# Performance work log

Hardware: AMD Instinct MI355X
Metric: run time of the kernel (lower is better)

The kernel has to match this reference:

```python
import jax, jax.numpy as jnp
import numpy as np

NT, NC, D = 20000, 80000, 256
SLOPE = 0.01  # torch F.leaky_relu default negative_slope


def _lrelu(x):
    return jnp.where(x >= 0, x, SLOPE * x)


def setup_inputs() -> dict:
    key = jax.random.key(0)
    ks = jax.random.split(key, 20)
    sc = 1.0 / np.sqrt(D)

    def W(k):
        return jax.random.normal(k, (D, D), jnp.float32) * sc

    return {
        "feat_table": jax.random.normal(ks[0], (NT, D), jnp.float32),
        "feat_column": jax.random.normal(ks[1], (NC, D), jnp.float32),
        "W_t2c": W(ks[2]), "b_t2c": jnp.zeros((D,), jnp.float32),
        "W_c2t": W(ks[3]), "b_c2t": jnp.zeros((D,), jnp.float32),
        "W_c2c": W(ks[4]), "b_c2c": jnp.zeros((D,), jnp.float32),
        "W_t2t": W(ks[5]), "b_t2t": jnp.zeros((D,), jnp.float32),
        "W_h": W(ks[6]), "b_h": jnp.zeros((D,), jnp.float32),
        "src_t2c": jax.random.randint(ks[7], (320000,), 0, NT, jnp.int32),
        "dst_t2c": jax.random.randint(ks[8], (320000,), 0, NC, jnp.int32),
        "src_c2t": jax.random.randint(ks[9], (320000,), 0, NC, jnp.int32),
        "dst_c2t": jax.random.randint(ks[10], (320000,), 0, NT, jnp.int32),
        "src_c2c": jax.random.randint(ks[11], (640000,), 0, NC, jnp.int32),
        "dst_c2c": jax.random.randint(ks[12], (640000,), 0, NC, jnp.int32),
        "src_t2t": jax.random.randint(ks[13], (160000,), 0, NT, jnp.int32),
        "dst_t2t": jax.random.randint(ks[14], (160000,), 0, NT, jnp.int32),
    }


def _mean_agg(Wh, src, dst, n_dst):
    # copy_u + mean: gather src messages, segment-mean into dst nodes
    s = jax.ops.segment_sum(Wh[src], dst, num_segments=n_dst)  # [n_dst, D]
    c = jax.ops.segment_sum(jnp.ones(src.shape, Wh.dtype), dst, num_segments=n_dst)
    return s / jnp.maximum(c, 1.0)[:, None]


def reference(feat_table, feat_column,
              W_t2c, b_t2c, W_c2t, b_c2t, W_c2c, b_c2c, W_t2t, b_t2t,
              W_h, b_h,
              src_t2c, dst_t2c, src_c2t, dst_c2t,
              src_c2c, dst_c2c, src_t2t, dst_t2t):
    # per-etype Linear + leaky_relu on source-node features
    Wh_t2c = _lrelu(feat_table @ W_t2c.T + b_t2c)
    Wh_c2t = _lrelu(feat_column @ W_c2t.T + b_c2t)
    Wh_c2c = _lrelu(feat_column @ W_c2c.T + b_c2c)
    Wh_t2t = _lrelu(feat_table @ W_t2t.T + b_t2t)

    # per-etype mean aggregation, then cross-etype 'mean' (2 etypes per ntype)
    h_table = 0.5 * (_mean_agg(Wh_c2t, src_c2t, dst_c2t, NT)
                     + _mean_agg(Wh_t2t, src_t2t, dst_t2t, NT))
    h_column = 0.5 * (_mean_agg(Wh_t2c, src_t2c, dst_t2c, NC)
                      + _mean_agg(Wh_c2c, src_c2c, dst_c2c, NC))

    out_table = _lrelu(h_table @ W_h.T + b_h) + feat_table
    out_column = _lrelu(h_column @ W_h.T + b_h) + feat_column
    return out_table, out_column
```

## Files before the change

kernel.cpp:

```cpp
#include <hip/hip_runtime.h>

#define D 256
#define SLOPE 0.01f

typedef __attribute__((ext_vector_type(8))) short bf16x8;
typedef __attribute__((ext_vector_type(4))) float f32x4;

__device__ __forceinline__ float bfbits2f(unsigned int hi) {
  return __builtin_bit_cast(float, hi);
}
__device__ __forceinline__ unsigned short f2bf(float f) {
  unsigned u = __builtin_bit_cast(unsigned, f);
  u += 0x7fffu + ((u >> 16) & 1u);
  return (unsigned short)(u >> 16);
}
__device__ __forceinline__ float lrelu(float x) {
  return (x >= 0.f) ? x : SLOPE * x;
}

__device__ __forceinline__ void gld_lds16(const void* g, void* l) {
  __builtin_amdgcn_global_load_lds(
      (const __attribute__((address_space(1))) unsigned int*)g,
      (__attribute__((address_space(3))) unsigned int*)l, 16, 0, 0);
}

__global__ void cast_kernel(const float* __restrict__ in,
                            unsigned short* __restrict__ out, int n4) {
  int i = blockIdx.x * blockDim.x + threadIdx.x;
  if (i >= n4) return;
  float4 v = ((const float4*)in)[i];
  ushort4 o;
  o.x = f2bf(v.x); o.y = f2bf(v.y); o.z = f2bf(v.z); o.w = f2bf(v.w);
  ((ushort4*)out)[i] = o;
}

__global__ void cast5_kernel(const float* w0, const float* w1, const float* w2,
                             const float* w3, const float* w4,
                             unsigned short* o0, unsigned short* o1,
                             unsigned short* o2, unsigned short* o3,
                             unsigned short* o4) {
  int a = blockIdx.y;
  const float* in = a == 0 ? w0 : a == 1 ? w1 : a == 2 ? w2 : a == 3 ? w3 : w4;
  unsigned short* out = a == 0 ? o0 : a == 1 ? o1 : a == 2 ? o2 : a == 3 ? o3 : o4;
  int i = blockIdx.x * blockDim.x + threadIdx.x;
  float4 v = ((const float4*)in)[i];
  ushort4 o;
  o.x = f2bf(v.x); o.y = f2bf(v.y); o.z = f2bf(v.z); o.w = f2bf(v.w);
  ((ushort4*)out)[i] = o;
}

template <int MODE>
__global__ __launch_bounds__(256, 2) void gemm_v2(
    const unsigned short* __restrict__ A, const unsigned short* __restrict__ B,
    const float* __restrict__ bias, const float* __restrict__ residual,
    unsigned short* __restrict__ outb, float* __restrict__ outf, int M) {
  __shared__ __attribute__((aligned(16))) unsigned short Xs[64 * 256];
  const int t = threadIdx.x;
  const int w = t >> 6, lane = t & 63;
  const int mblk = blockIdx.x * 64;
  const int fr = lane & 15;
  const int jb = lane >> 4;

  bf16x8 wf[4][8];
  {
    const unsigned short* wp =
        B + (size_t)(w * 64 + fr) * D + jb * 8;
#pragma unroll
    for (int nt = 0; nt < 4; nt++)
#pragma unroll
      for (int k0 = 0; k0 < 8; k0++)
        wf[nt][k0] = *(const bf16x8*)(wp + nt * 16 * D + k0 * 32);
  }

#pragma unroll
  for (int i = 0; i < 8; i++) {
    const int m = (i * 4 + w) * 2 + (lane >> 5);
    int row = mblk + m;
    if (row > M - 1) row = M - 1;
    const int jsrc = (lane & 31) ^ (m & 7);
    gld_lds16(A + (size_t)row * D + jsrc * 8, &Xs[(i * 4 + w) * 512]);
  }
  asm volatile("s_waitcnt vmcnt(0)" ::: "memory");
  __syncthreads();

  f32x4 acc[4][4];
#pragma unroll
  for (int i = 0; i < 4; i++)
#pragma unroll
    for (int j = 0; j < 4; j++) acc[i][j] = (f32x4){0.f, 0.f, 0.f, 0.f};

  const int r = fr & 7;
#pragma unroll
  for (int k0 = 0; k0 < 8; k0++) {
    bf16x8 xf[4];
#pragma unroll
    for (int mt = 0; mt < 4; mt++) {
      const int ml = mt * 16 + fr;
      xf[mt] = *(const bf16x8*)&Xs[ml * 256 + (((k0 * 4 + jb) ^ r) * 8)];
    }
#pragma unroll
    for (int mt = 0; mt < 4; mt++)
#pragma unroll
      for (int nt = 0; nt < 4; nt++)
        acc[mt][nt] = __builtin_amdgcn_mfma_f32_16x16x32_bf16(
            wf[nt][k0], xf[mt], acc[mt][nt], 0, 0, 0);
  }

  const int n0 = w * 64 + jb * 4;
  float4 bv[4];
#pragma unroll
  for (int nt = 0; nt < 4; nt++) bv[nt] = *(const float4*)&bias[n0 + nt * 16];

#pragma unroll
  for (int mt = 0; mt < 4; mt++) {
    const int m = mblk + mt * 16 + fr;
    if (m < M) {
      if (MODE == 1) {
        float4 rv[4];
#pragma unroll
        for (int nt = 0; nt < 4; nt++)
          rv[nt] = *(const float4*)&residual[(size_t)m * D + n0 + nt * 16];
#pragma unroll
        for (int nt = 0; nt < 4; nt++) {
          float4 o;
          o.x = lrelu(acc[mt][nt][0] + bv[nt].x) + rv[nt].x;
          o.y = lrelu(acc[mt][nt][1] + bv[nt].y) + rv[nt].y;
          o.z = lrelu(acc[mt][nt][2] + bv[nt].z) + rv[nt].z;
          o.w = lrelu(acc[mt][nt][3] + bv[nt].w) + rv[nt].w;
          *(float4*)&outf[(size_t)m * D + n0 + nt * 16] = o;
        }
      } else {
#pragma unroll
        for (int nt = 0; nt < 4; nt++) {
          ushort4 o;
          o.x = f2bf(lrelu(acc[mt][nt][0] + bv[nt].x));
          o.y = f2bf(lrelu(acc[mt][nt][1] + bv[nt].y));
          o.z = f2bf(lrelu(acc[mt][nt][2] + bv[nt].z));
          o.w = f2bf(lrelu(acc[mt][nt][3] + bv[nt].w));
          *(ushort4*)&outb[(size_t)m * D + n0 + nt * 16] = o;
        }
      }
    }
  }
}

__global__ void hist4_kernel(const int* d0, int n0, int* c0, const int* d1,
                             int n1, int* c1, const int* d2, int n2, int* c2,
                             const int* d3, int n3, int* c3) {
  int a = blockIdx.y;
  const int* dst = a == 0 ? d0 : a == 1 ? d1 : a == 2 ? d2 : d3;
  int n = a == 0 ? n0 : a == 1 ? n1 : a == 2 ? n2 : n3;
  int* cnt = a == 0 ? c0 : a == 1 ? c1 : a == 2 ? c2 : c3;
  int i = blockIdx.x * blockDim.x + threadIdx.x;
  if (i < n) atomicAdd(&cnt[dst[i]], 1);
}

__global__ __launch_bounds__(256) void scan_p1(
    const int* c0, int n0, const int* c1, int n1, const int* c2, int n2,
    const int* c3, int n3, int* __restrict__ bsum) {
  int a = blockIdx.y;
  const int* cnt = a == 0 ? c0 : a == 1 ? c1 : a == 2 ? c2 : c3;
  int n = a == 0 ? n0 : a == 1 ? n1 : a == 2 ? n2 : n3;
  int nblk = (n + 1023) >> 10;
  int blk = blockIdx.x;
  if (blk >= nblk) return;
  int t = threadIdx.x;
  int i = (blk << 10) + t * 4;
  int s = 0;
  if (i + 3 < n) {
    int4 v = *(const int4*)(cnt + i);
    s = v.x + v.y + v.z + v.w;
  } else {
#pragma unroll
    for (int j = 0; j < 4; j++)
      if (i + j < n) s += cnt[i + j];
  }
  __shared__ int red[256];
  red[t] = s;
  __syncthreads();
  for (int off = 128; off > 0; off >>= 1) {
    if (t < off) red[t] += red[t + off];
    __syncthreads();
  }
  if (t == 0) bsum[a * 128 + blk] = red[0];
}

__global__ __launch_bounds__(128) void scan_p2(int* __restrict__ bsum, int* o0,
                                               int n0, int* o1, int n1, int* o2,
                                               int n2, int* o3, int n3) {
  int a = blockIdx.x;
  int* offs = a == 0 ? o0 : a == 1 ? o1 : a == 2 ? o2 : o3;
  int n = a == 0 ? n0 : a == 1 ? n1 : a == 2 ? n2 : n3;
  int nblk = (n + 1023) >> 10;
  int t = threadIdx.x;
  int v = (t < nblk) ? bsum[a * 128 + t] : 0;
  __shared__ int s[128];
  s[t] = v;
  __syncthreads();
  for (int off = 1; off < 128; off <<= 1) {
    int u = (t >= off) ? s[t - off] : 0;
    __syncthreads();
    s[t] += u;
    __syncthreads();
  }
  if (t < nblk) bsum[a * 128 + t] = s[t] - v;
  if (t == 127) offs[n] = s[127];
}

__global__ __launch_bounds__(256) void scan_p3(
    const int* c0, int* o0, int n0, const int* c1, int* o1, int n1,
    const int* c2, int* o2, int n2, const int* c3, int* o3, int n3,
    const int* __restrict__ bsum) {
  int a = blockIdx.y;
  const int* cnt = a == 0 ? c0 : a == 1 ? c1 : a == 2 ? c2 : c3;
  int* offs = a == 0 ? o0 : a == 1 ? o1 : a == 2 ? o2 : o3;
  int n = a == 0 ? n0 : a == 1 ? n1 : a == 2 ? n2 : n3;
  int nblk = (n + 1023) >> 10;
  int blk = blockIdx.x;
  if (blk >= nblk) return;
  int t = threadIdx.x;
  int i = (blk << 10) + t * 4;
  int4 v = {0, 0, 0, 0};
  if (i + 3 < n) {
    v = *(const int4*)(cnt + i);
  } else {
    if (i < n) v.x = cnt[i];
    if (i + 1 < n) v.y = cnt[i + 1];
    if (i + 2 < n) v.z = cnt[i + 2];
    if (i + 3 < n) v.w = cnt[i + 3];
  }
  int s = v.x + v.y + v.z + v.w;
  __shared__ int sm[256];
  sm[t] = s;
  __syncthreads();
  for (int off = 1; off < 256; off <<= 1) {
    int u = (t >= off) ? sm[t - off] : 0;
    __syncthreads();
    sm[t] += u;
    __syncthreads();
  }
  int ex = sm[t] - s + bsum[a * 128 + blk];
  int4 o;
  o.x = ex;
  o.y = ex + v.x;
  o.z = ex + v.x + v.y;
  o.w = ex + v.x + v.y + v.z;
  if (i + 3 < n) {
    *(int4*)(offs + i) = o;
  } else {
    if (i < n) offs[i] = o.x;
    if (i + 1 < n) offs[i + 1] = o.y;
    if (i + 2 < n) offs[i + 2] = o.z;
    if (i + 3 < n) offs[i + 3] = o.w;
  }
}

__global__ void scatter4_kernel(
    const int* s0, const int* d0, int n0, const int* f0, int* u0, int* e0,
    const int* s1, const int* d1, int n1, const int* f1, int* u1, int* e1,
    const int* s2, const int* d2, int n2, const int* f2, int* u2, int* e2,
    const int* s3, const int* d3, int n3, const int* f3, int* u3, int* e3) {
  int a = blockIdx.y;
  const int* src = a == 0 ? s0 : a == 1 ? s1 : a == 2 ? s2 : s3;
  const int* dst = a == 0 ? d0 : a == 1 ? d1 : a == 2 ? d2 : d3;
  int n = a == 0 ? n0 : a == 1 ? n1 : a == 2 ? n2 : n3;
  const int* offs = a == 0 ? f0 : a == 1 ? f1 : a == 2 ? f2 : f3;
  int* cur = a == 0 ? u0 : a == 1 ? u1 : a == 2 ? u2 : u3;
  int* elist = a == 0 ? e0 : a == 1 ? e1 : a == 2 ? e2 : e3;
  int i = blockIdx.x * blockDim.x + threadIdx.x;
  if (i < n) {
    int d = dst[i];
    int p = offs[d] + atomicAdd(&cur[d], 1);
    elist[p] = src[i];
  }
}

__device__ __forceinline__ void add8(float* acc, uint4 p) {
  acc[0] += bfbits2f(p.x << 16);
  acc[1] += bfbits2f(p.x & 0xffff0000u);
  acc[2] += bfbits2f(p.y << 16);
  acc[3] += bfbits2f(p.y & 0xffff0000u);
  acc[4] += bfbits2f(p.z << 16);
  acc[5] += bfbits2f(p.z & 0xffff0000u);
  acc[6] += bfbits2f(p.w << 16);
  acc[7] += bfbits2f(p.w & 0xffff0000u);
}

__global__ __launch_bounds__(256) void aggregate_kernel(
    const unsigned short* __restrict__ WhA, const int* __restrict__ offsA,
    const int* __restrict__ elistA, const unsigned short* __restrict__ WhB,
    const int* __restrict__ offsB, const int* __restrict__ elistB,
    unsigned short* __restrict__ hout, int n) {
  int wave = (blockIdx.x * 256 + threadIdx.x) >> 6;
  int lane = threadIdx.x & 63;
  if (wave >= n) return;
  int half = lane >> 5;
  int l32 = lane & 31;
  size_t coff = (size_t)l32 * 8;

  float accA[8] = {0, 0, 0, 0, 0, 0, 0, 0};
  float accB[8] = {0, 0, 0, 0, 0, 0, 0, 0};
  float scA, scB;

  {
    int e0 = offsA[wave], e1 = offsA[wave + 1];
    scA = 0.5f / fmaxf((float)(e1 - e0), 1.0f);
    int e = e0;
    for (; e + 8 <= e1; e += 8) {
      int s0 = elistA[e + half];
      int s1 = elistA[e + 2 + half];
      int s2 = elistA[e + 4 + half];
      int s3 = elistA[e + 6 + half];
      uint4 p0 = *(const uint4*)(WhA + (size_t)s0 * D + coff);
      uint4 p1 = *(const uint4*)(WhA + (size_t)s1 * D + coff);
      uint4 p2 = *(const uint4*)(WhA + (size_t)s2 * D + coff);
      uint4 p3 = *(const uint4*)(WhA + (size_t)s3 * D + coff);
      add8(accA, p0); add8(accA, p1); add8(accA, p2); add8(accA, p3);
    }
    for (; e + 2 <= e1; e += 2) {
      int s0 = elistA[e + half];
      uint4 p0 = *(const uint4*)(WhA + (size_t)s0 * D + coff);
      add8(accA, p0);
    }
    if (e < e1 && half == 0) {
      int s0 = elistA[e];
      uint4 p0 = *(const uint4*)(WhA + (size_t)s0 * D + coff);
      add8(accA, p0);
    }
  }
  {
    int e0 = offsB[wave], e1 = offsB[wave + 1];
    scB = 0.5f / fmaxf((float)(e1 - e0), 1.0f);
    int e = e0;
    for (; e + 8 <= e1; e += 8) {
      int s0 = elistB[e + half];
      int s1 = elistB[e + 2 + half];
      int s2 = elistB[e + 4 + half];
      int s3 = elistB[e + 6 + half];
      uint4 p0 = *(const uint4*)(WhB + (size_t)s0 * D + coff);
      uint4 p1 = *(const uint4*)(WhB + (size_t)s1 * D + coff);
      uint4 p2 = *(const uint4*)(WhB + (size_t)s2 * D + coff);
      uint4 p3 = *(const uint4*)(WhB + (size_t)s3 * D + coff);
      add8(accB, p0); add8(accB, p1); add8(accB, p2); add8(accB, p3);
    }
    for (; e + 2 <= e1; e += 2) {
      int s0 = elistB[e + half];
      uint4 p0 = *(const uint4*)(WhB + (size_t)s0 * D + coff);
      add8(accB, p0);
    }
    if (e < e1 && half == 0) {
      int s0 = elistB[e];
      uint4 p0 = *(const uint4*)(WhB + (size_t)s0 * D + coff);
      add8(accB, p0);
    }
  }

  float h[8];
#pragma unroll
  for (int j = 0; j < 8; j++) {
    h[j] = accA[j] * scA + accB[j] * scB;
    h[j] += __shfl_down(h[j], 32);
  }
  if (half == 0) {
    uint4 o;
    o.x = (unsigned)f2bf(h[0]) | ((unsigned)f2bf(h[1]) << 16);
    o.y = (unsigned)f2bf(h[2]) | ((unsigned)f2bf(h[3]) << 16);
    o.z = (unsigned)f2bf(h[4]) | ((unsigned)f2bf(h[5]) << 16);
    o.w = (unsigned)f2bf(h[6]) | ((unsigned)f2bf(h[7]) << 16);
    *(uint4*)(hout + (size_t)wave * D + coff) = o;
  }
}

extern "C" void kernel_launch(void* const* d_in, const int* in_sizes, int n_in,
                              void* d_out, int out_size, void* d_ws,
                              size_t ws_size, hipStream_t stream) {
  const float* feat_table = (const float*)d_in[0];
  const float* feat_column = (const float*)d_in[1];
  const float* Wsrc[5] = {(const float*)d_in[2], (const float*)d_in[4],
                          (const float*)d_in[6], (const float*)d_in[8],
                          (const float*)d_in[10]};
  const float* b_t2c = (const float*)d_in[3];
  const float* b_c2t = (const float*)d_in[5];
  const float* b_c2c = (const float*)d_in[7];
  const float* b_t2t = (const float*)d_in[9];
  const float* b_h = (const float*)d_in[11];
  const int* src_t2c = (const int*)d_in[12];
  const int* dst_t2c = (const int*)d_in[13];
  const int* src_c2t = (const int*)d_in[14];
  const int* dst_c2t = (const int*)d_in[15];
  const int* src_c2c = (const int*)d_in[16];
  const int* dst_c2c = (const int*)d_in[17];
  const int* src_t2t = (const int*)d_in[18];
  const int* dst_t2t = (const int*)d_in[19];

  const int NT = in_sizes[0] / D;
  const int NC = in_sizes[1] / D;
  const int E_t2c = in_sizes[12], E_c2t = in_sizes[14];
  const int E_c2c = in_sizes[16], E_t2t = in_sizes[18];

  char* ws = (char*)d_ws;
  size_t cur = 0;
  auto alloc = [&](size_t bytes) -> void* {
    void* p = ws + cur;
    cur += (bytes + 255) & ~(size_t)255;
    return p;
  };
  unsigned short* Wb[5];
  for (int i = 0; i < 5; i++) Wb[i] = (unsigned short*)alloc((size_t)D * D * 2);
  unsigned short* ftb = (unsigned short*)alloc((size_t)NT * D * 2);
  unsigned short* fcb = (unsigned short*)alloc((size_t)NC * D * 2);
  unsigned short* Wh_t2c = (unsigned short*)alloc((size_t)NT * D * 2);
  unsigned short* Wh_c2t = (unsigned short*)alloc((size_t)NC * D * 2);
  unsigned short* Wh_c2c = (unsigned short*)alloc((size_t)NC * D * 2);
  unsigned short* Wh_t2t = (unsigned short*)alloc((size_t)NT * D * 2);
  unsigned short* h_tab = (unsigned short*)alloc((size_t)NT * D * 2);
  unsigned short* h_col = (unsigned short*)alloc((size_t)NC * D * 2);
  int* ints = (int*)alloc(sizeof(int) * 2 * (2 * (size_t)NT + 2 * (size_t)NC));
  int* cnt_c2t = ints;
  int* cnt_t2t = cnt_c2t + NT;
  int* cnt_t2c = cnt_t2t + NT;
  int* cnt_c2c = cnt_t2c + NC;
  int* cur_c2t = cnt_c2c + NC;
  int* cur_t2t = cur_c2t + NT;
  int* cur_t2c = cur_t2t + NT;
  int* cur_c2c = cur_t2c + NC;
  int* off_c2t = (int*)alloc(sizeof(int) * (NT + 1));
  int* off_t2t = (int*)alloc(sizeof(int) * (NT + 1));
  int* off_t2c = (int*)alloc(sizeof(int) * (NC + 1));
  int* off_c2c = (int*)alloc(sizeof(int) * (NC + 1));
  int* el_c2t = (int*)alloc(sizeof(int) * E_c2t);
  int* el_t2t = (int*)alloc(sizeof(int) * E_t2t);
  int* el_t2c = (int*)alloc(sizeof(int) * E_t2c);
  int* el_c2c = (int*)alloc(sizeof(int) * E_c2c);
  int* bsum = (int*)alloc(sizeof(int) * 4 * 128);

  hipMemsetAsync(ints, 0, sizeof(int) * 2 * (2 * (size_t)NT + 2 * (size_t)NC),
                 stream);

  {
    dim3 g((D * D / 4 + 255) / 256, 5);
    cast5_kernel<<<g, 256, 0, stream>>>(Wsrc[0], Wsrc[1], Wsrc[2], Wsrc[3],
                                        Wsrc[4], Wb[0], Wb[1], Wb[2], Wb[3],
                                        Wb[4]);
  }
  cast_kernel<<<((NT * D / 4) + 255) / 256, 256, 0, stream>>>(feat_table, ftb,
                                                              NT * D / 4);
  cast_kernel<<<((NC * D / 4) + 255) / 256, 256, 0, stream>>>(feat_column, fcb,
                                                              NC * D / 4);

  {
    dim3 g((NT + 63) / 64);
    gemm_v2<0><<<g, 256, 0, stream>>>(ftb, Wb[0], b_t2c, nullptr, Wh_t2c,
                                      nullptr, NT);
    gemm_v2<0><<<g, 256, 0, stream>>>(ftb, Wb[3], b_t2t, nullptr, Wh_t2t,
                                      nullptr, NT);
  }
  {
    dim3 g((NC + 63) / 64);
    gemm_v2<0><<<g, 256, 0, stream>>>(fcb, Wb[1], b_c2t, nullptr, Wh_c2t,
                                      nullptr, NC);
    gemm_v2<0><<<g, 256, 0, stream>>>(fcb, Wb[2], b_c2c, nullptr, Wh_c2c,
                                      nullptr, NC);
  }

  int Emax = max(max(E_c2t, E_t2t), max(E_t2c, E_c2c));
  {
    dim3 g((Emax + 255) / 256, 4);
    hist4_kernel<<<g, 256, 0, stream>>>(dst_c2t, E_c2t, cnt_c2t, dst_t2t,
                                        E_t2t, cnt_t2t, dst_t2c, E_t2c,
                                        cnt_t2c, dst_c2c, E_c2c, cnt_c2c);
  }
  int nmax = max(NT, NC);
  {
    dim3 g((nmax + 1023) / 1024, 4);
    scan_p1<<<g, 256, 0, stream>>>(cnt_c2t, NT, cnt_t2t, NT, cnt_t2c, NC,
                                   cnt_c2c, NC, bsum);
    scan_p2<<<4, 128, 0, stream>>>(bsum, off_c2t, NT, off_t2t, NT, off_t2c, NC,
                                   off_c2c, NC);
    scan_p3<<<g, 256, 0, stream>>>(cnt_c2t, off_c2t, NT, cnt_t2t, off_t2t, NT,
                                   cnt_t2c, off_t2c, NC, cnt_c2c, off_c2c, NC,
                                   bsum);
  }
  {
    dim3 g((Emax + 255) / 256, 4);
    scatter4_kernel<<<g, 256, 0, stream>>>(
        src_c2t, dst_c2t, E_c2t, off_c2t, cur_c2t, el_c2t, src_t2t, dst_t2t,
        E_t2t, off_t2t, cur_t2t, el_t2t, src_t2c, dst_t2c, E_t2c, off_t2c,
        cur_t2c, el_t2c, src_c2c, dst_c2c, E_c2c, off_c2c, cur_c2c, el_c2c);
  }

  aggregate_kernel<<<(NT + 3) / 4, 256, 0, stream>>>(
      Wh_c2t, off_c2t, el_c2t, Wh_t2t, off_t2t, el_t2t, h_tab, NT);
  aggregate_kernel<<<(NC + 3) / 4, 256, 0, stream>>>(
      Wh_t2c, off_t2c, el_t2c, Wh_c2c, off_c2c, el_c2c, h_col, NC);

  float* out_tab = (float*)d_out;
  float* out_col = out_tab + (size_t)NT * D;
  {
    dim3 g((NT + 63) / 64);
    gemm_v2<1><<<g, 256, 0, stream>>>(h_tab, Wb[4], b_h, feat_table, nullptr,
                                      out_tab, NT);
  }
  {
    dim3 g((NC + 63) / 64);
    gemm_v2<1><<<g, 256, 0, stream>>>(h_col, Wb[4], b_h, feat_column, nullptr,
                                      out_col, NC);
  }
}
```

Baseline: 620.0 us.

## Fuse feature cast into dual-weight GEMM and bucket edges before CSR scatter

The first-layer GEMMs now read fp32 features directly, convert them to bf16 in registers and write them to LDS. One 512-thread block computes both etype projections from the same input tile, which removes the separate cast kernels and the reload of the bf16 copy. The CSR edge scatter becomes a two-pass bucketed scheme: edges are first grouped into 512-node buckets using LDS counters, then scattered within each bucket. This localizes the global atomics and the elist writes, at the cost of an extra temp buffer and one more kernel launch.

```diff
diff --git a/kernel.cpp b/kernel.cpp
--- a/kernel.cpp
+++ b/kernel.cpp
@@ -2,6 +2,11 @@
 
 #define D 256
 #define SLOPE 0.01f
+
+#define BSH 9
+#define BSZ 512
+#define NBMAX 160
+#define EPB 8192
 
 typedef __attribute__((ext_vector_type(8))) short bf16x8;
 typedef __attribute__((ext_vector_type(4))) float f32x4;
@@ -22,16 +27,6 @@
   __builtin_amdgcn_global_load_lds(
       (const __attribute__((address_space(1))) unsigned int*)g,
       (__attribute__((address_space(3))) unsigned int*)l, 16, 0, 0);
-}
-
-__global__ void cast_kernel(const float* __restrict__ in,
-                            unsigned short* __restrict__ out, int n4) {
-  int i = blockIdx.x * blockDim.x + threadIdx.x;
-  if (i >= n4) return;
-  float4 v = ((const float4*)in)[i];
-  ushort4 o;
-  o.x = f2bf(v.x); o.y = f2bf(v.y); o.z = f2bf(v.z); o.w = f2bf(v.w);
-  ((ushort4*)out)[i] = o;
 }
 
 __global__ void cast5_kernel(const float* w0, const float* w1, const float* w2,
@@ -49,6 +44,104 @@
   ((ushort4*)out)[i] = o;
 }
 
+__global__ __launch_bounds__(512, 2) void gemm0_dual(
+    const float* __restrict__ Af, const unsigned short* __restrict__ B1,
+    const unsigned short* __restrict__ B2, const float* __restrict__ bias1,
+    const float* __restrict__ bias2, unsigned short* __restrict__ o1,
+    unsigned short* __restrict__ o2, int M) {
+  __shared__ __attribute__((aligned(16))) unsigned short Xs[64 * 256];
+  const int t = threadIdx.x;
+  const int wv = t >> 6, lane = t & 63;
+  const int half = wv >> 2;
+  const int w = wv & 3;
+  const int mblk = blockIdx.x * 64;
+  const int fr = lane & 15;
+  const int jb = lane >> 4;
+
+  const unsigned short* B = half ? B2 : B1;
+  const float* bias = half ? bias2 : bias1;
+  unsigned short* outb = half ? o2 : o1;
+
+  float4 v0[4], v1[4];
+  int cds[4];
+#pragma unroll
+  for (int i = 0; i < 4; i++) {
+    const int c = i * 512 + t;
+    const int m = c >> 5, jg = c & 31;
+    int row = mblk + m;
+    if (row > M - 1) row = M - 1;
+    const float* gp = Af + (size_t)row * D + jg * 8;
+    v0[i] = *(const float4*)gp;
+    v1[i] = *(const float4*)(gp + 4);
+    cds[i] = m * 32 + (jg ^ (m & 7));
+  }
+
+  bf16x8 wf[4][8];
+  {
+    const unsigned short* wp = B + (size_t)(w * 64 + fr) * D + jb * 8;
+#pragma unroll
+    for (int nt = 0; nt < 4; nt++)
+#pragma unroll
+      for (int k0 = 0; k0 < 8; k0++)
+        wf[nt][k0] = *(const bf16x8*)(wp + nt * 16 * D + k0 * 32);
+  }
+
+#pragma unroll
+  for (int i = 0; i < 4; i++) {
+    uint4 pk;
+    pk.x = (unsigned)f2bf(v0[i].x) | ((unsigned)f2bf(v0[i].y) << 16);
+    pk.y = (unsigned)f2bf(v0[i].z) | ((unsigned)f2bf(v0[i].w) << 16);
+    pk.z = (unsigned)f2bf(v1[i].x) | ((unsigned)f2bf(v1[i].y) << 16);
+    pk.w = (unsigned)f2bf(v1[i].z) | ((unsigned)f2bf(v1[i].w) << 16);
+    *(uint4*)&Xs[cds[i] * 8] = pk;
+  }
+  __syncthreads();
+
+  f32x4 acc[4][4];
+#pragma unroll
+  for (int i = 0; i < 4; i++)
+#pragma unroll
+    for (int j = 0; j < 4; j++) acc[i][j] = (f32x4){0.f, 0.f, 0.f, 0.f};
+
+  const int r = fr & 7;
+#pragma unroll
+  for (int k0 = 0; k0 < 8; k0++) {
+    bf16x8 xf[4];
+#pragma unroll
+    for (int mt = 0; mt < 4; mt++) {
+      const int ml = mt * 16 + fr;
+      xf[mt] = *(const bf16x8*)&Xs[ml * 256 + (((k0 * 4 + jb) ^ r) * 8)];
+    }
+#pragma unroll
+    for (int mt = 0; mt < 4; mt++)
+#pragma unroll
+      for (int nt = 0; nt < 4; nt++)
+        acc[mt][nt] = __builtin_amdgcn_mfma_f32_16x16x32_bf16(
+            wf[nt][k0], xf[mt], acc[mt][nt], 0, 0, 0);
+  }
+
+  const int n0 = w * 64 + jb * 4;
+  float4 bv[4];
+#pragma unroll
+  for (int nt = 0; nt < 4; nt++) bv[nt] = *(const float4*)&bias[n0 + nt * 16];
+
+#pragma unroll
+  for (int mt = 0; mt < 4; mt++) {
+    const int m = mblk + mt * 16 + fr;
+    if (m < M) {
+#pragma unroll
+      for (int nt = 0; nt < 4; nt++) {
+        ushort4 o;
+        o.x = f2bf(lrelu(acc[mt][nt][0] + bv[nt].x));
+        o.y = f2bf(lrelu(acc[mt][nt][1] + bv[nt].y));
+        o.z = f2bf(lrelu(acc[mt][nt][2] + bv[nt].z));
+        o.w = f2bf(lrelu(acc[mt][nt][3] + bv[nt].w));
+        *(ushort4*)&outb[(size_t)m * D + n0 + nt * 16] = o;
+      }
+    }
+  }
+}
+
 template <int MODE>
 __global__ __launch_bounds__(256, 2) void gemm_v2(
     const unsigned short* __restrict__ A, const unsigned short* __restrict__ B,
@@ -63,8 +156,7 @@
 
   bf16x8 wf[4][8];
   {
-    const unsigned short* wp =
-        B + (size_t)(w * 64 + fr) * D + jb * 8;
+    const unsigned short* wp = B + (size_t)(w * 64 + fr) * D + jb * 8;
 #pragma unroll
     for (int nt = 0; nt < 4; nt++)
 #pragma unroll
@@ -255,23 +347,85 @@
   }
 }
 
-__global__ void scatter4_kernel(
-    const int* s0, const int* d0, int n0, const int* f0, int* u0, int* e0,
-    const int* s1, const int* d1, int n1, const int* f1, int* u1, int* e1,
-    const int* s2, const int* d2, int n2, const int* f2, int* u2, int* e2,
-    const int* s3, const int* d3, int n3, const int* f3, int* u3, int* e3) {
+__global__ __launch_bounds__(256) void bucketA_kernel(
+    const int* s0, const int* d0, int n0, const int* f0, int* g0, unsigned* t0, int m0,
+    const int* s1, const int* d1, int n1, const int* f1, int* g1, unsigned* t1, int m1,
+    const int* s2, const int* d2, int n2, const int* f2, int* g2, unsigned* t2, int m2,
+    const int* s3, const int* d3, int n3, const int* f3, int* g3, unsigned* t3, int m3) {
   int a = blockIdx.y;
   const int* src = a == 0 ? s0 : a == 1 ? s1 : a == 2 ? s2 : s3;
   const int* dst = a == 0 ? d0 : a == 1 ? d1 : a == 2 ? d2 : d3;
   int n = a == 0 ? n0 : a == 1 ? n1 : a == 2 ? n2 : n3;
-  const int* offs = a == 0 ? f0 : a == 1 ? f1 : a == 2 ? f2 : f3;
+  const int* off = a == 0 ? f0 : a == 1 ? f1 : a == 2 ? f2 : f3;
+  int* bcur = a == 0 ? g0 : a == 1 ? g1 : a == 2 ? g2 : g3;
+  unsigned* temp = a == 0 ? t0 : a == 1 ? t1 : a == 2 ? t2 : t3;
+  int nn = a == 0 ? m0 : a == 1 ? m1 : a == 2 ? m2 : m3;
+
+  int blk = blockIdx.x;
+  if (blk * EPB >= n) return;
+  int nb = (nn + BSZ - 1) >> BSH;
+  int t = threadIdx.x;
+  __shared__ int cnt[NBMAX];
+  __shared__ int lbase[NBMAX];
+  if (t < NBMAX) cnt[t] = 0;
+  __syncthreads();
+
+  int i0 = blk * EPB + t;
+#pragma unroll 4
+  for (int it = 0; it < EPB / 256; it++) {
+    int i = i0 + it * 256;
+    if (i < n) atomicAdd(&cnt[dst[i] >> BSH], 1);
+  }
+  __syncthreads();
+  if (t < nb) {
+    int c = cnt[t];
+    int g = c ? atomicAdd(&bcur[t], c) : 0;
+    lbase[t] = g + off[t << BSH];
+    cnt[t] = 0;
+  }
+  __syncthreads();
+#pragma unroll 4
+  for (int it = 0; it < EPB / 256; it++) {
+    int i = i0 + it * 256;
+    if (i < n) {
+      int d = dst[i];
+      int b = d >> BSH;
+      int rk = atomicAdd(&cnt[b], 1);
+      temp[lbase[b] + rk] = ((unsigned)src[i] << BSH) | (unsigned)(d & (BSZ - 1));
+    }
+  }
+}
+
+__global__ __launch_bounds__(256) void bucketB_kernel(
+    const unsigned* t0, const int* f0, int* u0, int* e0, int m0,
+    const unsigned* t1, const int* f1, int* u1, int* e1, int m1,
+    const unsigned* t2, const int* f2, int* u2, int* e2, int m2,
+    const unsigned* t3, const int* f3, int* u3, int* e3, int m3) {
+  int a = blockIdx.y;
+  const unsigned* temp = a == 0 ? t0 : a == 1 ? t1 : a == 2 ? t2 : t3;
+  const int* off = a == 0 ? f0 : a == 1 ? f1 : a == 2 ? f2 : f3;
   int* cur = a == 0 ? u0 : a == 1 ? u1 : a == 2 ? u2 : u3;
   int* elist = a == 0 ? e0 : a == 1 ? e1 : a == 2 ? e2 : e3;
-  int i = blockIdx.x * blockDim.x + threadIdx.x;
-  if (i < n) {
-    int d = dst[i];
-    int p = offs[d] + atomicAdd(&cur[d], 1);
-    elist[p] = src[i];
+  int nn = a == 0 ? m0 : a == 1 ? m1 : a == 2 ? m2 : m3;
+
+  int nb = (nn + BSZ - 1) >> BSH;
+  int b = blockIdx.x >> 2, q = blockIdx.x & 3;
+  if (b >= nb) return;
+  int lo = off[b << BSH];
+  int hiIdx = (b + 1) << BSH;
+  if (hiIdx > nn) hiIdx = nn;
+  int hi = off[hiIdx];
+  int len = hi - lo;
+  int chunk = (len + 3) >> 2;
+  int st = lo + q * chunk;
+  int en = st + chunk;
+  if (en > hi) en = hi;
+  for (int i = st + threadIdx.x; i < en; i += 256) {
+    unsigned v = temp[i];
+    int d = (b << BSH) | (int)(v & (BSZ - 1));
+    int s = (int)(v >> BSH);
+    int p = off[d] + atomicAdd(&cur[d], 1);
+    elist[p] = s;
   }
 }
 
@@ -407,15 +561,14 @@
   };
   unsigned short* Wb[5];
   for (int i = 0; i < 5; i++) Wb[i] = (unsigned short*)alloc((size_t)D * D * 2);
-  unsigned short* ftb = (unsigned short*)alloc((size_t)NT * D * 2);
-  unsigned short* fcb = (unsigned short*)alloc((size_t)NC * D * 2);
   unsigned short* Wh_t2c = (unsigned short*)alloc((size_t)NT * D * 2);
   unsigned short* Wh_c2t = (unsigned short*)alloc((size_t)NC * D * 2);
   unsigned short* Wh_c2c = (unsigned short*)alloc((size_t)NC * D * 2);
   unsigned short* Wh_t2t = (unsigned short*)alloc((size_t)NT * D * 2);
   unsigned short* h_tab = (unsigned short*)alloc((size_t)NT * D * 2);
   unsigned short* h_col = (unsigned short*)alloc((size_t)NC * D * 2);
-  int* ints = (int*)alloc(sizeof(int) * 2 * (2 * (size_t)NT + 2 * (size_t)NC));
+  size_t nints = 2 * (2 * (size_t)NT + 2 * (size_t)NC) + 4 * NBMAX;
+  int* ints = (int*)alloc(sizeof(int) * nints);
   int* cnt_c2t = ints;
   int* cnt_t2t = cnt_c2t + NT;
   int* cnt_t2c = cnt_t2t + NT;
@@ -424,6 +577,10 @@
   int* cur_t2t = cur_c2t + NT;
   int* cur_t2c = cur_t2t + NT;
   int* cur_c2c = cur_t2c + NC;
+  int* bc_c2t = cur_c2c + NC;
+  int* bc_t2t = bc_c2t + NBMAX;
+  int* bc_t2c = bc_t2t + NBMAX;
+  int* bc_c2c = bc_t2c + NBMAX;
   int* off_c2t = (int*)alloc(sizeof(int) * (NT + 1));
   int* off_t2t = (int*)alloc(sizeof(int) * (NT + 1));
   int* off_t2c = (int*)alloc(sizeof(int) * (NC + 1));
@@ -432,10 +589,13 @@
   int* el_t2t = (int*)alloc(sizeof(int) * E_t2t);
   int* el_t2c = (int*)alloc(sizeof(int) * E_t2c);
   int* el_c2c = (int*)alloc(sizeof(int) * E_c2c);
+  unsigned* tp_c2t = (unsigned*)alloc(sizeof(unsigned) * E_c2t);
+  unsigned* tp_t2t = (unsigned*)alloc(sizeof(unsigned) * E_t2t);
+  unsigned* tp_t2c = (unsigned*)alloc(sizeof(unsigned) * E_t2c);
+  unsigned* tp_c2c = (unsigned*)alloc(sizeof(unsigned) * E_c2c);
   int* bsum = (int*)alloc(sizeof(int) * 4 * 128);
 
-  hipMemsetAsync(ints, 0, sizeof(int) * 2 * (2 * (size_t)NT + 2 * (size_t)NC),
-                 stream);
+  hipMemsetAsync(ints, 0, sizeof(int) * nints, stream);
 
   {
     dim3 g((D * D / 4 + 255) / 256, 5);
@@ -443,25 +603,11 @@
                                         Wsrc[4], Wb[0], Wb[1], Wb[2], Wb[3],
                                         Wb[4]);
   }
-  cast_kernel<<<((NT * D / 4) + 255) / 256, 256, 0, stream>>>(feat_table, ftb,
-                                                              NT * D / 4);
-  cast_kernel<<<((NC * D / 4) + 255) / 256, 256, 0, stream>>>(feat_column, fcb,
-                                                              NC * D / 4);
-
-  {
-    dim3 g((NT + 63) / 64);
-    gemm_v2<0><<<g, 256, 0, stream>>>(ftb, Wb[0], b_t2c, nullptr, Wh_t2c,
-                                      nullptr, NT);
-    gemm_v2<0><<<g, 256, 0, stream>>>(ftb, Wb[3], b_t2t, nullptr, Wh_t2t,
-                                      nullptr, NT);
-  }
-  {
-    dim3 g((NC + 63) / 64);
-    gemm_v2<0><<<g, 256, 0, stream>>>(fcb, Wb[1], b_c2t, nullptr, Wh_c2t,
-                                      nullptr, NC);
-    gemm_v2<0><<<g, 256, 0, stream>>>(fcb, Wb[2], b_c2c, nullptr, Wh_c2c,
-                                      nullptr, NC);
-  }
+
+  gemm0_dual<<<(NT + 63) / 64, 512, 0, stream>>>(
+      feat_table, Wb[0], Wb[3], b_t2c, b_t2t, Wh_t2c, Wh_t2t, NT);
+  gemm0_dual<<<(NC + 63) / 64, 512, 0, stream>>>(
+      feat_column, Wb[1], Wb[2], b_c2t, b_c2c, Wh_c2t, Wh_c2c, NC);
 
   int Emax = max(max(E_c2t, E_t2t), max(E_t2c, E_c2c));
   {
@@ -482,11 +628,21 @@
                                    bsum);
   }
   {
-    dim3 g((Emax + 255) / 256, 4);
-    scatter4_kernel<<<g, 256, 0, stream>>>(
-        src_c2t, dst_c2t, E_c2t, off_c2t, cur_c2t, el_c2t, src_t2t, dst_t2t,
-        E_t2t, off_t2t, cur_t2t, el_t2t, src_t2c, dst_t2c, E_t2c, off_t2c,
-        cur_t2c, el_t2c, src_c2c, dst_c2c, E_c2c, off_c2c, cur_c2c, el_c2c);
+    dim3 g((Emax + EPB - 1) / EPB, 4);
+    bucketA_kernel<<<g, 256, 0, stream>>>(
+        src_c2t, dst_c2t, E_c2t, off_c2t, bc_c2t, tp_c2t, NT,
+        src_t2t, dst_t2t, E_t2t, off_t2t, bc_t2t, tp_t2t, NT,
+        src_t2c, dst_t2c, E_t2c, off_t2c, bc_t2c, tp_t2c, NC,
+        src_c2c, dst_c2c, E_c2c, off_c2c, bc_c2c, tp_c2c, NC);
+  }
+  {
+    int nbmax = (max(NT, NC) + BSZ - 1) >> BSH;
+    dim3 g(nbmax * 4, 4);
+    bucketB_kernel<<<g, 256, 0, stream>>>(
+        tp_c2t, off_c2t, cur_c2t, el_c2t, NT,
+        tp_t2t, off_t2t, cur_t2t, el_t2t, NT,
+        tp_t2c, off_t2c, cur_t2c, el_t2c, NC,
+        tp_c2c, off_c2c, cur_c2c, el_c2c, NC);
   }
 
   aggregate_kernel<<<(NT + 3) / 4, 256, 0, stream>>>(
@@ -496,14 +652,8 @@
 
   float* out_tab = (float*)d_out;
   float* out_col = out_tab + (size_t)NT * D;
-  {
-    dim3 g((NT + 63) / 64);
-    gemm_v2<1><<<g, 256, 0, stream>>>(h_tab, Wb[4], b_h, feat_table, nullptr,
-                                      out_tab, NT);
-  }
-  {
-    dim3 g((NC + 63) / 64);
-    gemm_v2<1><<<g, 256, 0, stream>>>(h_col, Wb[4], b_h, feat_column, nullptr,
-                                      out_col, NC);
-  }
-}
+  gemm_v2<1><<<(NT + 63) / 64, 256, 0, stream>>>(h_tab, Wb[4], b_h, feat_table,
+                                                 nullptr, out_tab, NT);
+  gemm_v2<1><<<(NC + 63) / 64, 256, 0, stream>>>(h_col, Wb[4], b_h, feat_column,
+                                                 nullptr, out_col, NC);
+}
```

After: 623.4 us. Within noise of the previous version (+0.5%).
